# Optimization experiments

Measured on AMD Instinct MI355X. Metric: run time of the kernel, lower is better.

Reference implementation:

```python
import jax, jax.numpy as jnp
import numpy as np

N = 30000
E_RAND = 480000
NFEAT = 512
NHID = 64
NHEADS = 8
NCLASS = 500
ALPHA = 0.2


def setup_inputs() -> dict:
    key = jax.random.key(0)
    ks = jax.random.split(key, 8)
    features = jax.random.normal(ks[0], (N, NFEAT), dtype=jnp.float32)
    src = jax.random.randint(ks[1], (E_RAND,), 0, N, dtype=jnp.int32)
    dst = jax.random.randint(ks[2], (E_RAND,), 0, N, dtype=jnp.int32)
    loop = jnp.arange(N, dtype=jnp.int32)
    edge_index = jnp.stack([jnp.concatenate([src, loop]), jnp.concatenate([dst, loop])])  # [2, E]
    # xavier-normal-ish scaling keeps exp(-leakyrelu(.)) in a sane range
    W = jax.random.normal(ks[3], (NHEADS, NFEAT, NHID), dtype=jnp.float32) * (1.414 * np.sqrt(2.0 / (NFEAT + NHID)))
    a = jax.random.normal(ks[4], (NHEADS, 2 * NHID), dtype=jnp.float32) * (1.414 * np.sqrt(2.0 / (1 + 2 * NHID)))
    out_W = jax.random.normal(ks[5], (NHID * NHEADS, NCLASS), dtype=jnp.float32) * (1.414 * np.sqrt(2.0 / (NHID * NHEADS + NCLASS)))
    out_a = jax.random.normal(ks[6], (2 * NCLASS,), dtype=jnp.float32) * (1.414 * np.sqrt(2.0 / (1 + 2 * NCLASS)))
    return {"features": features, "edge_index": edge_index, "W": W, "a": a, "out_W": out_W, "out_a": out_a}


def _sp_gat_layer(x, W, a, src, dst, concat):
    # h = x @ W  -> [N, F']
    h = x @ W
    f = h.shape[1]
    n = x.shape[0]
    # a . cat(h[src], h[dst]) == (h @ a[:f])[src] + (h @ a[f:])[dst]  (avoids [E, 2F'] concat)
    s_src = h @ a[:f]
    s_dst = h @ a[f:]
    logits = s_src[src] + s_dst[dst]                      # [E]
    edge_e = jnp.exp(-jax.nn.leaky_relu(logits, negative_slope=ALPHA))
    # special_spmm(edge, edge_e, [N,N], ones)  -> per-row sum of attention values
    e_rowsum = jax.ops.segment_sum(edge_e, src, num_segments=n)        # [N]
    # special_spmm(edge, edge_e, [N,N], h)     -> attention-weighted neighbor sum
    h_prime = jax.ops.segment_sum(edge_e[:, None] * h[dst], src, num_segments=n)  # [N, F']
    h_prime = h_prime / e_rowsum[:, None]
    return jax.nn.elu(h_prime) if concat else h_prime


def reference(features, edge_index, W, a, out_W, out_a):
    src, dst = edge_index[0], edge_index[1]
    # multi-head sparse GAT (concat=True per head), python loop over fixed small head count
    heads = [_sp_gat_layer(features, W[i], a[i], src, dst, concat=True) for i in range(W.shape[0])]
    x = jnp.concatenate(heads, axis=1)                    # [N, nhid*nheads]
    out = jax.nn.elu(_sp_gat_layer(x, out_W, out_a, src, dst, concat=False))  # [N, nclass]
    return out
```

## Files before the change

kernel.cpp:

```cpp
#include <hip/hip_runtime.h>
#include <math.h>

typedef __attribute__((ext_vector_type(8))) short short8;
typedef __attribute__((ext_vector_type(4))) float f32x4;

#define NFEAT 512
#define HID_ALL 512
#define NCLASS 500
#define ALPHA 0.2f
#define BM 128
#define BN 128
#define DEGCAP 64

__device__ __forceinline__ ushort f32_to_bf16(float f) {
    union { float f; unsigned u; } v; v.f = f;
    unsigned u = v.u;
    unsigned r = (u + 0x7FFFu + ((u >> 16) & 1u)) >> 16;
    return (ushort)r;
}
__device__ __forceinline__ void unpack8(uint4 u, float* f) {
    f[0] = __uint_as_float(u.x << 16);
    f[1] = __uint_as_float(u.x & 0xFFFF0000u);
    f[2] = __uint_as_float(u.y << 16);
    f[3] = __uint_as_float(u.y & 0xFFFF0000u);
    f[4] = __uint_as_float(u.z << 16);
    f[5] = __uint_as_float(u.z & 0xFFFF0000u);
    f[6] = __uint_as_float(u.w << 16);
    f[7] = __uint_as_float(u.w & 0xFFFF0000u);
}
__device__ __forceinline__ float att_w(float lg) {
    return __expf(lg > 0.f ? -lg : -ALPHA * lg);
}
__device__ __forceinline__ void gload16(const void* g, void* l) {
    __builtin_amdgcn_global_load_lds(
        (const __attribute__((address_space(1))) unsigned int*)g,
        (__attribute__((address_space(3))) unsigned int*)l,
        16, 0, 0);
}

__global__ __launch_bounds__(256) void setup_kernel(const float* __restrict__ W,
                                                    ushort* __restrict__ W1T,
                                                    const float* __restrict__ oW,
                                                    ushort* __restrict__ W2T,
                                                    const float* __restrict__ oa,
                                                    float* __restrict__ oas,
                                                    float* __restrict__ oad,
                                                    int* __restrict__ cnt,
                                                    float* __restrict__ s2, float* __restrict__ d2,
                                                    int N) {
    __shared__ float tile[64][65];
    int bid = blockIdx.x;
    if (bid < 64) {
        int head = bid >> 3;
        int f0 = (bid & 7) << 6;
        int tx = threadIdx.x & 63, tyb = threadIdx.x >> 6;
        const float* Wh = W + ((size_t)head << 15);
#pragma unroll
        for (int r = 0; r < 16; r++) {
            int ty = (tyb << 4) + r;
            tile[ty][tx] = Wh[(size_t)(f0 + ty) * 64 + tx];
        }
        __syncthreads();
#pragma unroll
        for (int r = 0; r < 16; r++) {
            int ty = (tyb << 4) + r;
            W1T[(size_t)((head << 6) + ty) * 512 + f0 + tx] = f32_to_bf16(tile[tx][ty]);
        }
    } else if (bid < 128) {
        int b = bid - 64;
        int f0 = (b >> 3) << 6;
        int c0 = (b & 7) << 6;
        int tx = threadIdx.x & 63, tyb = threadIdx.x >> 6;
#pragma unroll
        for (int r = 0; r < 16; r++) {
            int ty = (tyb << 4) + r;
            int c = c0 + tx;
            tile[ty][tx] = (c < NCLASS) ? oW[(size_t)(f0 + ty) * NCLASS + c] : 0.f;
        }
        __syncthreads();
#pragma unroll
        for (int r = 0; r < 16; r++) {
            int ty = (tyb << 4) + r;
            W2T[(size_t)(c0 + ty) * 512 + f0 + tx] = f32_to_bf16(tile[tx][ty]);
        }
    } else {
        int idx = (bid - 128) * 256 + threadIdx.x;
        if (idx < 512) {
            oas[idx] = (idx < NCLASS) ? oa[idx] : 0.f;
            oad[idx] = (idx < NCLASS) ? oa[NCLASS + idx] : 0.f;
        }
        if (idx < N) { cnt[idx] = 0; s2[idx] = 0.f; d2[idx] = 0.f; }
    }
}

__global__ void scatter_kernel(const int* __restrict__ src, const int* __restrict__ dst,
                               int* __restrict__ cnt, int* __restrict__ colidx, int E) {
    int e = blockIdx.x * blockDim.x + threadIdx.x;
    if (e >= E) return;
    int s = src[e];
    int p = (s << 6) + atomicAdd(&cnt[s], 1);
    colidx[p] = dst[e];
}

template <int MODE, int AF32>
__global__ __launch_bounds__(256) void gemm_fused_kernel(const ushort* __restrict__ A16,
                                                         const float* __restrict__ A32,
                                                         const ushort* __restrict__ Bt,
                                                         ushort* __restrict__ C,
                                                         const float* __restrict__ av,
                                                         const float* __restrict__ av2,
                                                         float* __restrict__ sv,
                                                         float* __restrict__ dv,
                                                         int M) {
    __shared__ ushort As[BM * 64];
    __shared__ ushort Bs[BN * 64];
    int m0 = blockIdx.x * BM;
    int n0 = blockIdx.y * BN;
    int t = threadIdx.x;
    int lane = t & 63, wid = t >> 6;
    int wr = wid >> 1, wc = wid & 1;
    int g = lane >> 4, r15 = lane & 15;
    int srow = lane >> 3;
    int schunk = lane & 7;
    f32x4 acc[4][4] = {};
    for (int k0 = 0; k0 < 512; k0 += 64) {
        __syncthreads();
#pragma unroll
        for (int j = 0; j < 4; j++) {
            int rb = j * 32 + wid * 8;
            int r = rb + srow;
            int rowA = m0 + r; if (rowA >= M) rowA = M - 1;
            if (AF32) {
                const float* srcp = &A32[(size_t)rowA * 512 + k0 + (schunk << 3)];
                float4 p0 = *reinterpret_cast<const float4*>(srcp);
                float4 p1 = *reinterpret_cast<const float4*>(srcp + 4);
                short8 vv;
                vv[0] = (short)f32_to_bf16(p0.x); vv[1] = (short)f32_to_bf16(p0.y);
                vv[2] = (short)f32_to_bf16(p0.z); vv[3] = (short)f32_to_bf16(p0.w);
                vv[4] = (short)f32_to_bf16(p1.x); vv[5] = (short)f32_to_bf16(p1.y);
                vv[6] = (short)f32_to_bf16(p1.z); vv[7] = (short)f32_to_bf16(p1.w);
                *reinterpret_cast<short8*>(&As[r * 64 + ((schunk ^ (srow & 7)) << 3)]) = vv;
            } else {
                int ca = (schunk ^ (srow & 7)) << 3;
                gload16(&A16[(size_t)rowA * 512 + k0 + ca], &As[rb * 64]);
            }
            int rowB = n0 + r;
            int cb = (schunk ^ (srow & 7)) << 3;
            gload16(&Bt[(size_t)rowB * 512 + k0 + cb], &Bs[rb * 64]);
        }
        __syncthreads();
#pragma unroll
        for (int kk = 0; kk < 2; kk++) {
            int coff = ((kk * 4 + g) ^ (r15 & 7)) << 3;
            short8 af[4], bfr[4];
#pragma unroll
            for (int mi = 0; mi < 4; mi++)
                af[mi] = *reinterpret_cast<const short8*>(&As[((wr << 6) + mi * 16 + r15) * 64 + coff]);
#pragma unroll
            for (int ni = 0; ni < 4; ni++)
                bfr[ni] = *reinterpret_cast<const short8*>(&Bs[((wc << 6) + ni * 16 + r15) * 64 + coff]);
#pragma unroll
            for (int mi = 0; mi < 4; mi++)
#pragma unroll
                for (int ni = 0; ni < 4; ni++)
                    acc[mi][ni] = __builtin_amdgcn_mfma_f32_16x16x32_bf16(af[mi], bfr[ni], acc[mi][ni], 0, 0, 0);
        }
    }
    int fr = g << 2;
    int col = r15;
#pragma unroll
    for (int mi = 0; mi < 4; mi++)
#pragma unroll
        for (int ni = 0; ni < 4; ni++)
#pragma unroll
            for (int r = 0; r < 4; r++) {
                int grow = m0 + (wr << 6) + mi * 16 + fr + r;
                if (grow < M) {
                    int gcol = n0 + (wc << 6) + ni * 16 + col;
                    C[(size_t)grow * 512 + gcol] = f32_to_bf16(acc[mi][ni][r]);
                }
            }
    float ws[4], wd[4];
    int h = (n0 >> 6) + wc;
#pragma unroll
    for (int ni = 0; ni < 4; ni++) {
        if (MODE == 0) {
            int k = ni * 16 + col;
            ws[ni] = av[(h << 7) + k];
            wd[ni] = av[(h << 7) + 64 + k];
        } else {
            int gcol = n0 + (wc << 6) + ni * 16 + col;
            ws[ni] = av[gcol];
            wd[ni] = av2[gcol];
        }
    }
#pragma unroll
    for (int mi = 0; mi < 4; mi++)
#pragma unroll
        for (int r = 0; r < 4; r++) {
            float ps = 0.f, pd = 0.f;
#pragma unroll
            for (int ni = 0; ni < 4; ni++) {
                float v = acc[mi][ni][r];
                ps += v * ws[ni];
                pd += v * wd[ni];
            }
#pragma unroll
            for (int off = 1; off < 16; off <<= 1) {
                ps += __shfl_xor(ps, off);
                pd += __shfl_xor(pd, off);
            }
            int grow = m0 + (wr << 6) + mi * 16 + fr + r;
            if (col == 0 && grow < M) {
                if (MODE == 0) {
                    sv[(grow << 3) + h] = ps;
                    dv[(grow << 3) + h] = pd;
                } else {
                    atomicAdd(&sv[grow], ps);
                    atomicAdd(&dv[grow], pd);
                }
            }
        }
}

#define LOAD4_1(C0,C1,C2,C3,G0,G1,G2,G3,U0,U1,U2,U3,ii)                                  \
    C0 = colidx[ii]; C1 = colidx[ii + 1]; C2 = colidx[ii + 2]; C3 = colidx[ii + 3];      \
    G0 = d1[(C0 << 3) + h]; G1 = d1[(C1 << 3) + h];                                      \
    G2 = d1[(C2 << 3) + h]; G3 = d1[(C3 << 3) + h];                                      \
    U0 = *reinterpret_cast<const uint4*>(&h1[(size_t)C0 * 512 + lane * 8]);              \
    U1 = *reinterpret_cast<const uint4*>(&h1[(size_t)C1 * 512 + lane * 8]);              \
    U2 = *reinterpret_cast<const uint4*>(&h1[(size_t)C2 * 512 + lane * 8]);              \
    U3 = *reinterpret_cast<const uint4*>(&h1[(size_t)C3 * 512 + lane * 8]);

#define CONS4(G0,G1,G2,G3,U0,U1,U2,U3)                                                   \
    {                                                                                    \
        float w0 = att_w(sn + G0), w1 = att_w(sn + G1);                                  \
        float w2 = att_w(sn + G2), w3 = att_w(sn + G3);                                  \
        rsum += (w0 + w1) + (w2 + w3);                                                   \
        float f[8];                                                                      \
        unpack8(U0, f);                                                                  \
        _Pragma("unroll") for (int q = 0; q < 8; q++) acc[q] += w0 * f[q];               \
        unpack8(U1, f);                                                                  \
        _Pragma("unroll") for (int q = 0; q < 8; q++) acc[q] += w1 * f[q];               \
        unpack8(U2, f);                                                                  \
        _Pragma("unroll") for (int q = 0; q < 8; q++) acc[q] += w2 * f[q];               \
        unpack8(U3, f);                                                                  \
        _Pragma("unroll") for (int q = 0; q < 8; q++) acc[q] += w3 * f[q];               \
    }

__global__ __launch_bounds__(256) void agg1_kernel(const ushort* __restrict__ h1,
                                                   const float* __restrict__ s1,
                                                   const float* __restrict__ d1,
                                                   const int* __restrict__ cnt,
                                                   const int* __restrict__ colidx,
                                                   ushort* __restrict__ x, int N) {
    int lane = threadIdx.x & 63;
    int n = (blockIdx.x << 2) + (threadIdx.x >> 6);
    if (n >= N) return;
    int h = lane >> 3;
    float sn = s1[(n << 3) + h];
    float acc[8] = {0.f, 0.f, 0.f, 0.f, 0.f, 0.f, 0.f, 0.f};
    float rsum = 0.f;
    int beg = n << 6, end = beg + cnt[n];
    int i = beg;
    {
        int ac0, ac1, ac2, ac3, bc0, bc1, bc2, bc3;
        float ag0, ag1, ag2, ag3, bg0, bg1, bg2, bg3;
        uint4 au0, au1, au2, au3, bu0, bu1, bu2, bu3;
        if (i + 4 <= end) {
            LOAD4_1(ac0, ac1, ac2, ac3, ag0, ag1, ag2, ag3, au0, au1, au2, au3, i);
            i += 4;
            while (i + 4 <= end) {
                LOAD4_1(bc0, bc1, bc2, bc3, bg0, bg1, bg2, bg3, bu0, bu1, bu2, bu3, i);
                i += 4;
                CONS4(ag0, ag1, ag2, ag3, au0, au1, au2, au3);
                if (i + 4 <= end) {
                    LOAD4_1(ac0, ac1, ac2, ac3, ag0, ag1, ag2, ag3, au0, au1, au2, au3, i);
                    i += 4;
                    CONS4(bg0, bg1, bg2, bg3, bu0, bu1, bu2, bu3);
                } else {
                    CONS4(bg0, bg1, bg2, bg3, bu0, bu1, bu2, bu3);
                    goto tail1;
                }
            }
            CONS4(ag0, ag1, ag2, ag3, au0, au1, au2, au3);
        }
    }
tail1:
    for (; i < end; i++) {
        int dv = colidx[i];
        float w = att_w(sn + d1[(dv << 3) + h]);
        rsum += w;
        uint4 u = *reinterpret_cast<const uint4*>(&h1[(size_t)dv * 512 + lane * 8]);
        float f[8]; unpack8(u, f);
#pragma unroll
        for (int q = 0; q < 8; q++) acc[q] += w * f[q];
    }
    float inv = 1.f / rsum;
    uint ov[4];
#pragma unroll
    for (int p = 0; p < 4; p++) {
        float v0 = acc[2 * p] * inv;     v0 = v0 > 0.f ? v0 : __expf(v0) - 1.f;
        float v1 = acc[2 * p + 1] * inv; v1 = v1 > 0.f ? v1 : __expf(v1) - 1.f;
        ov[p] = (uint)f32_to_bf16(v0) | ((uint)f32_to_bf16(v1) << 16);
    }
    uint4 o; o.x = ov[0]; o.y = ov[1]; o.z = ov[2]; o.w = ov[3];
    *reinterpret_cast<uint4*>(&x[(size_t)n * 512 + lane * 8]) = o;
}

#define LOAD4_2(C0,C1,C2,C3,G0,G1,G2,G3,U0,U1,U2,U3,ii)                                  \
    C0 = colidx[ii]; C1 = colidx[ii + 1]; C2 = colidx[ii + 2]; C3 = colidx[ii + 3];      \
    G0 = d2[C0]; G1 = d2[C1]; G2 = d2[C2]; G3 = d2[C3];                                  \
    U0 = *reinterpret_cast<const uint4*>(&h2[(size_t)C0 * 512 + c0]);                    \
    U1 = *reinterpret_cast<const uint4*>(&h2[(size_t)C1 * 512 + c0]);                    \
    U2 = *reinterpret_cast<const uint4*>(&h2[(size_t)C2 * 512 + c0]);                    \
    U3 = *reinterpret_cast<const uint4*>(&h2[(size_t)C3 * 512 + c0]);

__global__ __launch_bounds__(256) void agg2_kernel(const ushort* __restrict__ h2,
                                                   const float* __restrict__ s2,
                                                   const float* __restrict__ d2,
                                                   const int* __restrict__ cnt,
                                                   const int* __restrict__ colidx,
                                                   float* __restrict__ out, int N) {
    int lane = threadIdx.x & 63;
    int n = (blockIdx.x << 2) + (threadIdx.x >> 6);
    if (n >= N) return;
    int c0 = lane * 8;
    float sn = s2[n];
    float acc[8] = {0.f, 0.f, 0.f, 0.f, 0.f, 0.f, 0.f, 0.f};
    float rsum = 0.f;
    int beg = n << 6, end = beg + cnt[n];
    int i = beg;
    {
        int ac0, ac1, ac2, ac3, bc0, bc1, bc2, bc3;
        float ag0, ag1, ag2, ag3, bg0, bg1, bg2, bg3;
        uint4 au0, au1, au2, au3, bu0, bu1, bu2, bu3;
        if (i + 4 <= end) {
            LOAD4_2(ac0, ac1, ac2, ac3, ag0, ag1, ag2, ag3, au0, au1, au2, au3, i);
            i += 4;
            while (i + 4 <= end) {
                LOAD4_2(bc0, bc1, bc2, bc3, bg0, bg1, bg2, bg3, bu0, bu1, bu2, bu3, i);
                i += 4;
                CONS4(ag0, ag1, ag2, ag3, au0, au1, au2, au3);
                if (i + 4 <= end) {
                    LOAD4_2(ac0, ac1, ac2, ac3, ag0, ag1, ag2, ag3, au0, au1, au2, au3, i);
                    i += 4;
                    CONS4(bg0, bg1, bg2, bg3, bu0, bu1, bu2, bu3);
                } else {
                    CONS4(bg0, bg1, bg2, bg3, bu0, bu1, bu2, bu3);
                    goto tail2;
                }
            }
            CONS4(ag0, ag1, ag2, ag3, au0, au1, au2, au3);
        }
    }
tail2:
    for (; i < end; i++) {
        int dv = colidx[i];
        float w = att_w(sn + d2[dv]);
        rsum += w;
        uint4 u = *reinterpret_cast<const uint4*>(&h2[(size_t)dv * 512 + c0]);
        float f[8]; unpack8(u, f);
#pragma unroll
        for (int q = 0; q < 8; q++) acc[q] += w * f[q];
    }
    float inv = 1.f / rsum;
#pragma unroll
    for (int q = 0; q < 8; q++) {
        int c = c0 + q;
        if (c < NCLASS) {
            float v = acc[q] * inv;
            v = v > 0.f ? v : __expf(v) - 1.f;
            out[(size_t)n * NCLASS + c] = v;
        }
    }
}

extern "C" void kernel_launch(void* const* d_in, const int* in_sizes, int n_in,
                              void* d_out, int out_size, void* d_ws, size_t ws_size,
                              hipStream_t stream) {
    const float* features = (const float*)d_in[0];
    const int* edge_index = (const int*)d_in[1];
    const float* W = (const float*)d_in[2];
    const float* a = (const float*)d_in[3];
    const float* out_W = (const float*)d_in[4];
    const float* out_a = (const float*)d_in[5];
    float* out = (float*)d_out;

    int N = in_sizes[0] / NFEAT;
    int E = in_sizes[1] / 2;
    const int* src = edge_index;
    const int* dst = edge_index + E;

    char* base = (char*)d_ws;
    size_t off = 0;
    auto alloc = [&](size_t bytes) -> char* {
        char* r = base + off;
        off += (bytes + 255) & ~(size_t)255;
        return r;
    };
    ushort* h1b   = (ushort*)alloc((size_t)N * 512 * 2);
    ushort* xb    = (ushort*)alloc((size_t)N * 512 * 2);
    ushort* h2b   = h1b;
    ushort* w1t   = (ushort*)alloc(512 * 512 * 2);
    ushort* w2t   = (ushort*)alloc(512 * 512 * 2);
    float* s1 = (float*)alloc((size_t)N * 8 * 4);
    float* d1 = (float*)alloc((size_t)N * 8 * 4);
    float* s2 = (float*)alloc((size_t)N * 4);
    float* d2 = (float*)alloc((size_t)N * 4);
    float* oas = (float*)alloc(512 * 4);
    float* oad = (float*)alloc(512 * 4);
    int* colidx = (int*)alloc((size_t)N * DEGCAP * 4);
    int* cnt = (int*)alloc((size_t)N * 4);
    if (off > ws_size) return;

    int zblocks = (N + 255) / 256;
    setup_kernel<<<128 + zblocks, 256, 0, stream>>>(W, w1t, out_W, w2t, out_a, oas, oad,
                                                    cnt, s2, d2, N);
    scatter_kernel<<<(E + 255) / 256, 256, 0, stream>>>(src, dst, cnt, colidx, E);

    dim3 gemm_grid((N + BM - 1) / BM, HID_ALL / BN);
    gemm_fused_kernel<0, 1><<<gemm_grid, 256, 0, stream>>>(nullptr, features, w1t, h1b,
                                                           a, nullptr, s1, d1, N);
    agg1_kernel<<<(N + 3) / 4, 256, 0, stream>>>(h1b, s1, d1, cnt, colidx, xb, N);
    gemm_fused_kernel<1, 0><<<gemm_grid, 256, 0, stream>>>(xb, nullptr, w2t, h2b,
                                                           oas, oad, s2, d2, N);
    agg2_kernel<<<(N + 3) / 4, 256, 0, stream>>>(h2b, s2, d2, cnt, colidx, out, N);
}
```

Measured before the change: 283.3 us.

## Double-buffer GEMM shared-memory tiles with k-step 32 to overlap loads and MFMA

Restructures the fused GEMM main loop to use two shared-memory buffers of half the K depth (32 instead of 64). The next tile is staged while MFMAs run on the current one, leaving one barrier per iteration instead of two. The LDS swizzle is changed to a 4-chunk XOR pattern to fit the narrower tile. The aim is to hide global-load latency behind compute. In exchange there are twice as many iterations, each doing less work, and the f32 path still converts data in registers before the current tile's compute.

Result: slower. 293.0 us (+3.4%).

```diff
diff --git a/kernel.cpp b/kernel.cpp
--- a/kernel.cpp
+++ b/kernel.cpp
@@ -112,60 +112,74 @@
                                                          float* __restrict__ sv,
                                                          float* __restrict__ dv,
                                                          int M) {
-    __shared__ ushort As[BM * 64];
-    __shared__ ushort Bs[BN * 64];
+    __shared__ ushort As[2 * BM * 32];
+    __shared__ ushort Bs[2 * BM * 32];
     int m0 = blockIdx.x * BM;
     int n0 = blockIdx.y * BN;
     int t = threadIdx.x;
     int lane = t & 63, wid = t >> 6;
     int wr = wid >> 1, wc = wid & 1;
     int g = lane >> 4, r15 = lane & 15;
-    int srow = lane >> 3;
-    int schunk = lane & 7;
+    int srow = lane >> 2;
+    int schunk = lane & 3;
+    int skey = (srow ^ (srow >> 2)) & 3;
+    int rkey = (r15 ^ (r15 >> 2)) & 3;
     f32x4 acc[4][4] = {};
-    for (int k0 = 0; k0 < 512; k0 += 64) {
+
+#define STAGE_TILE(buf, kof)                                                              \
+    {                                                                                     \
+        _Pragma("unroll")                                                                 \
+        for (int j = 0; j < 2; j++) {                                                     \
+            int rb = j * 64 + wid * 16;                                                   \
+            int r = rb + srow;                                                            \
+            int ca = (schunk ^ skey) << 3;                                                \
+            int rowA = m0 + r; if (rowA >= M) rowA = M - 1;                               \
+            if (AF32) {                                                                   \
+                const float* srcp = &A32[(size_t)rowA * 512 + (kof) + ca];                \
+                float4 p0 = *reinterpret_cast<const float4*>(srcp);                       \
+                float4 p1 = *reinterpret_cast<const float4*>(srcp + 4);                   \
+                short8 vv;                                                                \
+                vv[0] = (short)f32_to_bf16(p0.x); vv[1] = (short)f32_to_bf16(p0.y);       \
+                vv[2] = (short)f32_to_bf16(p0.z); vv[3] = (short)f32_to_bf16(p0.w);       \
+                vv[4] = (short)f32_to_bf16(p1.x); vv[5] = (short)f32_to_bf16(p1.y);       \
+                vv[6] = (short)f32_to_bf16(p1.z); vv[7] = (short)f32_to_bf16(p1.w);       \
+                *reinterpret_cast<short8*>(&As[(buf) * (BM * 32) + r * 32 + (schunk << 3)]) = vv; \
+            } else {                                                                      \
+                gload16(&A16[(size_t)rowA * 512 + (kof) + ca],                            \
+                        &As[(buf) * (BM * 32) + rb * 32]);                                \
+            }                                                                             \
+            int rowB = n0 + r;                                                            \
+            gload16(&Bt[(size_t)rowB * 512 + (kof) + ca],                                 \
+                    &Bs[(buf) * (BM * 32) + rb * 32]);                                    \
+        }                                                                                 \
+    }
+
+    STAGE_TILE(0, 0);
+    __syncthreads();
+    int cur = 0;
+#pragma unroll
+    for (int it = 0; it < 16; ++it) {
+        if (it + 1 < 16) STAGE_TILE(cur ^ 1, (it + 1) * 32);
+        int coff = ((g ^ rkey) << 3);
+        short8 af[4], bfr[4];
+#pragma unroll
+        for (int mi = 0; mi < 4; mi++)
+            af[mi] = *reinterpret_cast<const short8*>(
+                &As[cur * (BM * 32) + ((wr << 6) + mi * 16 + r15) * 32 + coff]);
+#pragma unroll
+        for (int ni = 0; ni < 4; ni++)
+            bfr[ni] = *reinterpret_cast<const short8*>(
+                &Bs[cur * (BM * 32) + ((wc << 6) + ni * 16 + r15) * 32 + coff]);
+#pragma unroll
+        for (int mi = 0; mi < 4; mi++)
+#pragma unroll
+            for (int ni = 0; ni < 4; ni++)
+                acc[mi][ni] = __builtin_amdgcn_mfma_f32_16x16x32_bf16(af[mi], bfr[ni], acc[mi][ni], 0, 0, 0);
         __syncthreads();
-#pragma unroll
-        for (int j = 0; j < 4; j++) {
-            int rb = j * 32 + wid * 8;
-            int r = rb + srow;
-            int rowA = m0 + r; if (rowA >= M) rowA = M - 1;
-            if (AF32) {
-                const float* srcp = &A32[(size_t)rowA * 512 + k0 + (schunk << 3)];
-                float4 p0 = *reinterpret_cast<const float4*>(srcp);
-                float4 p1 = *reinterpret_cast<const float4*>(srcp + 4);
-                short8 vv;
-                vv[0] = (short)f32_to_bf16(p0.x); vv[1] = (short)f32_to_bf16(p0.y);
-                vv[2] = (short)f32_to_bf16(p0.z); vv[3] = (short)f32_to_bf16(p0.w);
-                vv[4] = (short)f32_to_bf16(p1.x); vv[5] = (short)f32_to_bf16(p1.y);
-                vv[6] = (short)f32_to_bf16(p1.z); vv[7] = (short)f32_to_bf16(p1.w);
-                *reinterpret_cast<short8*>(&As[r * 64 + ((schunk ^ (srow & 7)) << 3)]) = vv;
-            } else {
-                int ca = (schunk ^ (srow & 7)) << 3;
-                gload16(&A16[(size_t)rowA * 512 + k0 + ca], &As[rb * 64]);
-            }
-            int rowB = n0 + r;
-            int cb = (schunk ^ (srow & 7)) << 3;
-            gload16(&Bt[(size_t)rowB * 512 + k0 + cb], &Bs[rb * 64]);
-        }
-        __syncthreads();
-#pragma unroll
-        for (int kk = 0; kk < 2; kk++) {
-            int coff = ((kk * 4 + g) ^ (r15 & 7)) << 3;
-            short8 af[4], bfr[4];
-#pragma unroll
-            for (int mi = 0; mi < 4; mi++)
-                af[mi] = *reinterpret_cast<const short8*>(&As[((wr << 6) + mi * 16 + r15) * 64 + coff]);
-#pragma unroll
-            for (int ni = 0; ni < 4; ni++)
-                bfr[ni] = *reinterpret_cast<const short8*>(&Bs[((wc << 6) + ni * 16 + r15) * 64 + coff]);
-#pragma unroll
-            for (int mi = 0; mi < 4; mi++)
-#pragma unroll
-                for (int ni = 0; ni < 4; ni++)
-                    acc[mi][ni] = __builtin_amdgcn_mfma_f32_16x16x32_bf16(af[mi], bfr[ni], acc[mi][ni], 0, 0, 0);
-        }
-    }
+        cur ^= 1;
+    }
+#undef STAGE_TILE
+
     int fr = g << 2;
     int col = r15;
 #pragma unroll
```
